# Performance work log

Measured on AMD Instinct MI355X. Metric: run time of the kernel, lower is better.

The kernel has to match this reference:

```python
import jax, jax.numpy as jnp
import numpy as np
import math

CTX_LEN = 2048
N_EMB = 256
HEAD_SIZE = 256
N_HEADS = 8
HEAD_DIM = HEAD_SIZE // N_HEADS  # 32
B, T = 4, 2048


def setup_inputs() -> dict:
    key = jax.random.key(0)
    k1, k2, k3, k4 = jax.random.split(key, 4)
    x = jax.random.normal(k1, (B, T, N_EMB), dtype=jnp.float32)
    # torch Linear(n_emb, 3*head_size, bias=False): store as [in, out] for x @ W
    w_attn = jax.random.normal(k2, (N_EMB, 3 * HEAD_SIZE), dtype=jnp.float32) * 0.02
    pos_embs = jax.random.normal(k3, (N_HEADS, CTX_LEN, HEAD_DIM), dtype=jnp.float32) * 0.02
    w_proj = jax.random.normal(k4, (HEAD_SIZE, N_EMB), dtype=jnp.float32) * 0.02
    b_proj = jnp.zeros((N_EMB,), dtype=jnp.float32)
    return {"x": x, "w_attn": w_attn, "pos_embs": pos_embs,
            "w_proj": w_proj, "b_proj": b_proj}


def reference(x, w_attn, pos_embs, w_proj, b_proj):
    Bsz, Tlen, _ = x.shape
    qkv = x @ w_attn                               # [B,T,3*HS]
    K, Q, V = jnp.split(qkv, 3, axis=-1)           # split order: K, Q, V (as in source)
    def heads(t):                                  # [B,T,HS] -> [B,H,T,hd]
        return t.reshape(Bsz, Tlen, N_HEADS, HEAD_DIM).transpose(0, 2, 1, 3)
    K, Q, V = heads(K), heads(Q), heads(V)

    # relative position term with skew trick
    pe = pos_embs[:, -Tlen:, :]                    # [H,T,hd]
    S_rel = jnp.einsum('bhtd,hsd->bhts', Q, pe)    # [B,H,T,T]
    flip_mask = jnp.flip(jnp.tril(jnp.ones((Tlen, Tlen), dtype=x.dtype)), axis=1)
    S_rel = S_rel * flip_mask
    # pad a zero column at the front, reshape [T+1,T], drop first row -> skew
    S_rel = jnp.pad(S_rel, ((0, 0), (0, 0), (0, 0), (1, 0)))
    S_rel = S_rel.reshape(Bsz, N_HEADS, Tlen + 1, Tlen)[:, :, 1:, :]

    scores = (jnp.einsum('bhtd,bhsd->bhts', Q, K) + S_rel) / math.sqrt(HEAD_DIM)
    causal = jnp.where(jnp.tril(jnp.ones((Tlen, Tlen), dtype=bool)), 0.0, -1e9).astype(x.dtype)
    scores = scores + causal
    attn = jax.nn.softmax(scores, axis=-1)         # dropout omitted (eval mode)

    out = jnp.einsum('bhts,bhsd->bhtd', attn, V)   # [B,H,T,hd]
    out = out.transpose(0, 2, 1, 3).reshape(Bsz, Tlen, HEAD_SIZE)
    return out @ w_proj + b_proj
```

## Files before the change

kernel.cpp:

```cpp
#include <hip/hip_runtime.h>
#include <math.h>

#define BB 4
#define TT 2048
#define TTP 2112
#define NEMB 256
#define NH 8
#define HD 32

typedef __attribute__((ext_vector_type(8))) short bf8;
typedef __attribute__((ext_vector_type(4))) float f4;

static __device__ __forceinline__ unsigned short f2bf(float f) {
    union { float f; unsigned u; } v; v.f = f;
    unsigned r = v.u + 0x7FFF + ((v.u >> 16) & 1);
    return (unsigned short)(r >> 16);
}
static __device__ __forceinline__ float bf2f(unsigned short s) {
    union { unsigned u; float f; } v; v.u = ((unsigned)s) << 16;
    return v.f;
}

template <int CTRL>
static __device__ __forceinline__ float dppmv(float x) {
    return __int_as_float(__builtin_amdgcn_mov_dpp(__float_as_int(x), CTRL, 0xF, 0xF, true));
}
static __device__ __forceinline__ float rowsum16(float x) {
    x += dppmv<0xB1>(x);
    x += dppmv<0x4E>(x);
    x += dppmv<0x124>(x);
    x += dppmv<0x128>(x);
    return x;
}

static __device__ __forceinline__ void tcvt_body(const float* __restrict__ src,
                                                 unsigned short* __restrict__ dst,
                                                 int R, int C, int gx, int gy,
                                                 float (*t)[65], int tid) {
    const int c0 = gx * 64, r0 = gy * 64;
    #pragma unroll
    for (int p = 0; p < 4; ++p) {
        const int i = tid + p * 256;
        const int r = i >> 4, c4 = (i & 15) * 4;
        const float4 v = *(const float4*)(src + (long)(r0 + r) * C + c0 + c4);
        t[r][c4] = v.x; t[r][c4+1] = v.y; t[r][c4+2] = v.z; t[r][c4+3] = v.w;
    }
    __syncthreads();
    #pragma unroll
    for (int p = 0; p < 4; ++p) {
        const int i = tid + p * 256;
        const int cr = i >> 4, r4 = (i & 15) * 4;
        ushort4 vv;
        vv.x = f2bf(t[r4+0][cr]); vv.y = f2bf(t[r4+1][cr]);
        vv.z = f2bf(t[r4+2][cr]); vv.w = f2bf(t[r4+3][cr]);
        *(ushort4*)(dst + (long)(c0 + cr) * R + r0 + r4) = vv;
    }
}

__global__ __launch_bounds__(256) void prep(const float* __restrict__ pe,
                                            unsigned short* __restrict__ peb,
                                            const float* __restrict__ wa,
                                            unsigned short* __restrict__ waT,
                                            const float* __restrict__ wp,
                                            unsigned short* __restrict__ wpT) {
    __shared__ float t[64][65];
    const int bx = blockIdx.x, tid = threadIdx.x;
    if (bx < 528) {
        const int idx4 = bx * 256 + tid;
        const int h   = idx4 / 16896;
        const int rem = idx4 - h * 16896;
        const int u   = rem >> 3;
        const int d4  = (rem & 7) * 4;
        ushort4 o = make_ushort4(0, 0, 0, 0);
        if (u < TT) {
            const float4 v = *(const float4*)(pe + ((long)(h * TT + u)) * HD + d4);
            o.x = f2bf(v.x); o.y = f2bf(v.y); o.z = f2bf(v.z); o.w = f2bf(v.w);
        }
        *(ushort4*)(peb + ((long)(h * TTP + u)) * HD + d4) = o;
    } else if (bx < 576) {
        const int lo = bx - 528;
        tcvt_body(wa, waT, 256, 768, lo % 12, lo / 12, t, tid);
    } else {
        const int lo = bx - 576;
        tcvt_body(wp, wpT, 256, 256, lo % 4, lo / 4, t, tid);
    }
}

__global__ __launch_bounds__(256) void qkv_mfma(const float* __restrict__ xg,
                                                const unsigned short* __restrict__ Bg,
                                                unsigned short* __restrict__ Kb,
                                                unsigned short* __restrict__ Qb,
                                                unsigned short* __restrict__ Vt) {
    __shared__ unsigned short sm[13824];
    unsigned short* As = sm;
    unsigned short* Bs = sm + 9216;
    const int tid = threadIdx.x;
    const int wv = tid >> 6, L = tid & 63;
    const int l15 = L & 15, q = L >> 4;
    const int n0 = blockIdx.x * 64;
    const int m0 = blockIdx.y * 128;

    f4 acc[2][4];
    #pragma unroll
    for (int mt = 0; mt < 2; ++mt)
        #pragma unroll
        for (int nt = 0; nt < 4; ++nt) acc[mt][nt] = (f4){0.f,0.f,0.f,0.f};

    for (int kc = 0; kc < 4; ++kc) {
        const int k0 = kc * 64;
        __syncthreads();
        #pragma unroll
        for (int p = 0; p < 4; ++p) {
            const int i = tid + p * 256;
            const int r = i >> 3, c = i & 7;
            const float4 va = *(const float4*)(xg + (long)(m0 + r) * 256 + k0 + c * 8);
            const float4 vb = *(const float4*)(xg + (long)(m0 + r) * 256 + k0 + c * 8 + 4);
            ushort4 lo, hi;
            lo.x = f2bf(va.x); lo.y = f2bf(va.y); lo.z = f2bf(va.z); lo.w = f2bf(va.w);
            hi.x = f2bf(vb.x); hi.y = f2bf(vb.y); hi.z = f2bf(vb.z); hi.w = f2bf(vb.w);
            *(ushort4*)(As + r * 72 + c * 8)     = lo;
            *(ushort4*)(As + r * 72 + c * 8 + 4) = hi;
        }
        #pragma unroll
        for (int p = 0; p < 2; ++p) {
            const int i = tid + p * 256;
            const int r = i >> 3, c = i & 7;
            *(bf8*)(Bs + r * 72 + c * 8) = *(const bf8*)(Bg + (long)(n0 + r) * 256 + k0 + c * 8);
        }
        __syncthreads();
        #pragma unroll
        for (int kk = 0; kk < 2; ++kk) {
            const bf8 a0 = *(const bf8*)(As + (wv * 32 + l15) * 72 + kk * 32 + q * 8);
            const bf8 a1 = *(const bf8*)(As + (wv * 32 + 16 + l15) * 72 + kk * 32 + q * 8);
            #pragma unroll
            for (int nt = 0; nt < 4; ++nt) {
                const bf8 bb = *(const bf8*)(Bs + (nt * 16 + l15) * 72 + kk * 32 + q * 8);
                acc[0][nt] = __builtin_amdgcn_mfma_f32_16x16x32_bf16(a0, bb, acc[0][nt], 0, 0, 0);
                acc[1][nt] = __builtin_amdgcn_mfma_f32_16x16x32_bf16(a1, bb, acc[1][nt], 0, 0, 0);
            }
        }
    }

    const int sec = n0 >> 8;
    #pragma unroll
    for (int mt = 0; mt < 2; ++mt) {
        const int gm = m0 + wv * 32 + mt * 16 + q * 4;
        const int b = gm >> 11, tb = gm & 2047;
        #pragma unroll
        for (int nt = 0; nt < 4; ++nt) {
            const int gn = n0 + nt * 16 + l15;
            const int cc = gn & 255, h = cc >> 5, d = cc & 31;
            const long bh = (long)b * NH + h;
            const f4 a = acc[mt][nt];
            if (sec == 2) {
                ushort4 vv;
                vv.x = f2bf(a[0]); vv.y = f2bf(a[1]); vv.z = f2bf(a[2]); vv.w = f2bf(a[3]);
                *(ushort4*)(Vt + (bh * HD + d) * TT + tb) = vv;
            } else if (sec == 1) {
                #pragma unroll
                for (int r = 0; r < 4; ++r)
                    Qb[(bh * TT + tb + r) * HD + d] = f2bf(a[r] * 0.25506655788696527f);
            } else {
                #pragma unroll
                for (int r = 0; r < 4; ++r)
                    Kb[(bh * TT + tb + r) * HD + d] = f2bf(a[r]);
            }
        }
    }
}

__global__ __launch_bounds__(256) void attn_kernel(const unsigned short* __restrict__ Kb,
                                                   const unsigned short* __restrict__ Qb,
                                                   const unsigned short* __restrict__ Vtg,
                                                   const unsigned short* __restrict__ peb,
                                                   unsigned short* __restrict__ po,
                                                   float* __restrict__ pl) {
    __shared__ unsigned short lds[14592];
    unsigned short* Ks  = lds;
    unsigned short* PEs = lds + 2560;
    unsigned short* Vts = lds + 7680;
    unsigned short* Psw = lds + 9984 + (threadIdx.x >> 6) * 1152;

    const int tid = threadIdx.x;
    const int wv  = tid >> 6;
    const int L   = tid & 63;
    const int l15 = L & 15;
    const int q   = L >> 4;
    const int pair = blockIdx.x >> 1;
    const int sblk = blockIdx.x & 1;
    const int h = blockIdx.y, b = blockIdx.z;
    const long bh = (long)b * NH + h;
    const unsigned short* Kg = Kb  + bh * TT * HD;
    const unsigned short* Qg = Qb  + bh * TT * HD;
    const unsigned short* Vg = Vtg + bh * HD * TT;
    const unsigned short* Pg = peb + (long)h * TTP * HD;

    const int krow = tid >> 2, kc = tid & 3;
    const int vrow = tid >> 3, vc = tid & 7;
    const f4 z4 = {0.f, 0.f, 0.f, 0.f};
    const f4 m4 = {-16.f, -16.f, -16.f, -16.f};

    int saddr[4]; unsigned psel[4];
    #pragma unroll
    for (int r = 0; r < 4; ++r) {
        const int tcol = l15 + 15 - 4 * q - r;
        saddr[r] = ((q << 4) | (tcol & 15)) << 2;
        psel[r]  = (tcol < 16) ? 0x01000C0Cu : 0x03020C0Cu;
    }

    for (int half = 0; half < 2; ++half) {
        const int itile = half ? 31 - pair : pair;
        const int t0 = itile * 64;

        const bf8 aq = *(const bf8*)(Qg + (t0 + wv * 16 + l15) * HD + q * 8);
        f4 o0 = z4, o1 = z4;
        float l_st[4] = {0.f, 0.f, 0.f, 0.f};

        for (int jt = sblk; jt <= itile; jt += 2) {
            const int s0 = jt * 64;
            const int ubase = TT - 64 - t0 + s0;
            __syncthreads();
            *(bf8*)(Ks  + krow * 40 + kc * 8) = *(const bf8*)(Kg + (s0 + krow) * HD + kc * 8);
            *(bf8*)(Vts + vrow * 72 + vc * 8) = *(const bf8*)(Vg + vrow * TT + s0 + vc * 8);
            #pragma unroll
            for (int kk = 0; kk < 2; ++kk) {
                const int i  = tid + kk * 256;
                const int pr = i >> 2, pc = i & 3;
                *(bf8*)(PEs + pr * 40 + pc * 8) = *(const bf8*)(Pg + (long)(ubase + pr) * HD + pc * 8);
            }
            __syncthreads();

            f4 sa[4], ra[5];
            #pragma unroll
            for (int nt = 0; nt < 4; ++nt) {
                const bf8 bk = *(const bf8*)(Ks + (nt * 16 + l15) * 40 + q * 8);
                sa[nt] = __builtin_amdgcn_mfma_f32_16x16x32_bf16(aq, bk, m4, 0, 0, 0);
            }
            const int pebase = 48 - 16 * wv;
            #pragma unroll
            for (int nt = 0; nt < 5; ++nt) {
                const bf8 bp = *(const bf8*)(PEs + (pebase + nt * 16 + l15) * 40 + q * 8);
                ra[nt] = __builtin_amdgcn_mfma_f32_16x16x32_bf16(aq, bp, z4, 0, 0, 0);
            }

            #pragma unroll
            for (int nb = 0; nb < 4; ++nb) {
                #pragma unroll
                for (int r = 0; r < 4; ++r) {
                    const unsigned packed = __builtin_amdgcn_perm(
                        (unsigned)__float_as_int(ra[nb + 1][r]),
                        (unsigned)__float_as_int(ra[nb][r]), 0x07060302u);
                    const int v = __builtin_amdgcn_ds_bpermute(saddr[r], (int)packed);
                    const unsigned sel = __builtin_amdgcn_perm((unsigned)v, (unsigned)v, psel[r]);
                    sa[nb][r] += __int_as_float((int)sel);
                }
            }

            if (jt == itile) {
                #pragma unroll
                for (int nb = 0; nb < 4; ++nb)
                    #pragma unroll
                    for (int r = 0; r < 4; ++r) {
                        const int s_l = nb * 16 + l15;
                        const int t_l = wv * 16 + 4 * q + r;
                        if (s_l > t_l) sa[nb][r] = -1e30f;
                    }
            }

            #pragma unroll
            for (int r = 0; r < 4; ++r) {
                #pragma unroll
                for (int nb = 0; nb < 4; ++nb) {
                    const float p = exp2f(sa[nb][r]);
                    l_st[r] += p;
                    const unsigned pu = (unsigned)__float_as_int(p);
                    Psw[(4 * q + r) * 72 + nb * 16 + l15] =
                        (unsigned short)((pu + 0x8000u) >> 16);
                }
            }

            #pragma unroll
            for (int ks = 0; ks < 2; ++ks) {
                const bf8 ap  = *(const bf8*)(Psw + l15 * 72 + ks * 32 + q * 8);
                const bf8 bv0 = *(const bf8*)(Vts + l15 * 72 + ks * 32 + q * 8);
                const bf8 bv1 = *(const bf8*)(Vts + (16 + l15) * 72 + ks * 32 + q * 8);
                o0 = __builtin_amdgcn_mfma_f32_16x16x32_bf16(ap, bv0, o0, 0, 0, 0);
                o1 = __builtin_amdgcn_mfma_f32_16x16x32_bf16(ap, bv1, o1, 0, 0, 0);
            }
        }

        const long pt = (bh * 32 + itile) * 2 + sblk;
        unsigned short* pob = po + pt * 2048;
        #pragma unroll
        for (int r = 0; r < 4; ++r) {
            const int row = wv * 16 + 4 * q + r;
            pob[row * 32 + l15]      = f2bf(o0[r]);
            pob[row * 32 + 16 + l15] = f2bf(o1[r]);
            const float ls = rowsum16(l_st[r]);
            if (l15 == 0) pl[pt * 64 + row] = ls;
        }
    }
}

__global__ __launch_bounds__(256) void attn_merge(const unsigned short* __restrict__ po,
                                                  const float* __restrict__ pl,
                                                  unsigned short* __restrict__ attb) {
    const int i = blockIdx.x * 256 + threadIdx.x;
    const int d4   = i & 7;
    const int row  = (i >> 3) & 63;
    const int tile = (i >> 9) & 31;
    const int bh   = i >> 14;
    const int h = bh & 7, b = bh >> 3;
    const long pt0 = ((long)bh * 32 + tile) * 2;
    const float l0 = pl[pt0 * 64 + row], l1 = pl[(pt0 + 1) * 64 + row];
    const float inv = 1.0f / (l0 + l1);
    const ushort4 a = *(const ushort4*)(po + pt0 * 2048 + row * 32 + d4 * 4);
    const ushort4 c = *(const ushort4*)(po + (pt0 + 1) * 2048 + row * 32 + d4 * 4);
    ushort4 o;
    o.x = f2bf((bf2f(a.x) + bf2f(c.x)) * inv);
    o.y = f2bf((bf2f(a.y) + bf2f(c.y)) * inv);
    o.z = f2bf((bf2f(a.z) + bf2f(c.z)) * inv);
    o.w = f2bf((bf2f(a.w) + bf2f(c.w)) * inv);
    const int t = tile * 64 + row;
    *(ushort4*)(attb + ((long)(b * TT + t)) * NEMB + h * HD + d4 * 4) = o;
}

__global__ __launch_bounds__(256) void proj_mfma(const unsigned short* __restrict__ Ag,
                                                 const unsigned short* __restrict__ Bg,
                                                 const float* __restrict__ bias,
                                                 float* __restrict__ out) {
    __shared__ unsigned short sm[13824];
    unsigned short* As = sm;
    unsigned short* Bs = sm + 9216;
    const int tid = threadIdx.x;
    const int wv = tid >> 6, L = tid & 63;
    const int l15 = L & 15, q = L >> 4;
    const int n0 = blockIdx.x * 64;
    const int m0 = blockIdx.y * 128;

    f4 acc[2][4];
    #pragma unroll
    for (int mt = 0; mt < 2; ++mt)
        #pragma unroll
        for (int nt = 0; nt < 4; ++nt) acc[mt][nt] = (f4){0.f,0.f,0.f,0.f};

    for (int kc = 0; kc < 4; ++kc) {
        const int k0 = kc * 64;
        __syncthreads();
        #pragma unroll
        for (int p = 0; p < 4; ++p) {
            const int i = tid + p * 256;
            const int r = i >> 3, c = i & 7;
            *(bf8*)(As + r * 72 + c * 8) = *(const bf8*)(Ag + (long)(m0 + r) * 256 + k0 + c * 8);
        }
        #pragma unroll
        for (int p = 0; p < 2; ++p) {
            const int i = tid + p * 256;
            const int r = i >> 3, c = i & 7;
            *(bf8*)(Bs + r * 72 + c * 8) = *(const bf8*)(Bg + (long)(n0 + r) * 256 + k0 + c * 8);
        }
        __syncthreads();
        #pragma unroll
        for (int kk = 0; kk < 2; ++kk) {
            const bf8 a0 = *(const bf8*)(As + (wv * 32 + l15) * 72 + kk * 32 + q * 8);
            const bf8 a1 = *(const bf8*)(As + (wv * 32 + 16 + l15) * 72 + kk * 32 + q * 8);
            #pragma unroll
            for (int nt = 0; nt < 4; ++nt) {
                const bf8 bb = *(const bf8*)(Bs + (nt * 16 + l15) * 72 + kk * 32 + q * 8);
                acc[0][nt] = __builtin_amdgcn_mfma_f32_16x16x32_bf16(a0, bb, acc[0][nt], 0, 0, 0);
                acc[1][nt] = __builtin_amdgcn_mfma_f32_16x16x32_bf16(a1, bb, acc[1][nt], 0, 0, 0);
            }
        }
    }

    #pragma unroll
    for (int mt = 0; mt < 2; ++mt) {
        const int gm = m0 + wv * 32 + mt * 16 + q * 4;
        #pragma unroll
        for (int nt = 0; nt < 4; ++nt) {
            const int gn = n0 + nt * 16 + l15;
            const float bv = bias[gn];
            #pragma unroll
            for (int r = 0; r < 4; ++r)
                out[(long)(gm + r) * NEMB + gn] = acc[mt][nt][r] + bv;
        }
    }
}

extern "C" void kernel_launch(void* const* d_in, const int* in_sizes, int n_in,
                              void* d_out, int out_size, void* d_ws, size_t ws_size,
                              hipStream_t stream) {
    const float* x      = (const float*)d_in[0];
    const float* w_attn = (const float*)d_in[1];
    const float* pe     = (const float*)d_in[2];
    const float* w_proj = (const float*)d_in[3];
    const float* b_proj = (const float*)d_in[4];
    float* out = (float*)d_out;

    char* base = (char*)d_ws;
    unsigned short* Kb   = (unsigned short*)(base);
    unsigned short* Qb   = (unsigned short*)(base + ( 4u << 20));
    unsigned short* Vt   = (unsigned short*)(base + ( 8u << 20));
    unsigned short* attb = (unsigned short*)(base + (12u << 20));
    unsigned short* peb  = (unsigned short*)(base + (16u << 20));
    unsigned short* waT  = (unsigned short*)(base + (18u << 20));
    unsigned short* wpT  = (unsigned short*)(base + (37u << 19));
    unsigned short* po   = (unsigned short*)(base + (19u << 20));
    float*          pl   = (float*)        (base + (27u << 20));

    prep<<<dim3(592), 256, 0, stream>>>(pe, peb, w_attn, waT, w_proj, wpT);
    qkv_mfma<<<dim3(12, 64), 256, 0, stream>>>(x, waT, Kb, Qb, Vt);
    attn_kernel<<<dim3(32, NH, BB), 256, 0, stream>>>(Kb, Qb, Vt, peb, po, pl);
    attn_merge<<<dim3(2048), 256, 0, stream>>>(po, pl, attb);
    proj_mfma<<<dim3(4, 64), 256, 0, stream>>>(attb, wpT, b_proj, out);
}
```

Measured before the change: 153.8 us.

## Process both paired query tiles in one KV sweep, sharing K/V tile loads

The attention kernel now handles its two query tiles (pair and 31-pair) in a single loop over key tiles instead of two sequential passes. Each K/V tile is loaded into LDS once and used by both query tiles, with a separate positional-embedding buffer for each. This halves K/V global loads and the number of barrier-separated iterations. The skew shuffle is also reworked to issue 3 ds_bpermute per row instead of 4, and the P scratch stride changes from 72 to 76. The cost is more LDS per block and extra registers for the second set of accumulators, which may reduce occupancy.

```diff
diff --git a/kernel.cpp b/kernel.cpp
--- a/kernel.cpp
+++ b/kernel.cpp
@@ -169,17 +169,83 @@
     }
 }
 
+
+static __device__ __forceinline__ void finish_tile(
+    f4* sa, const bf8 aq, const unsigned short* __restrict__ PEs,
+    unsigned short* __restrict__ Psw, bool diag,
+    const bf8 bv00, const bf8 bv01, const bf8 bv10, const bf8 bv11,
+    f4& o0, f4& o1, float* l_st,
+    const int* saddr, const unsigned* pselL, const unsigned* pselX,
+    int wv, int l15, int q)
+{
+    const f4 z4 = {0.f, 0.f, 0.f, 0.f};
+    const int pebase = 48 - 16 * wv;
+    f4 ra[5];
+    #pragma unroll
+    for (int nt = 0; nt < 5; ++nt) {
+        const bf8 bp = *(const bf8*)(PEs + (pebase + nt * 16 + l15) * 40 + q * 8);
+        ra[nt] = __builtin_amdgcn_mfma_f32_16x16x32_bf16(aq, bp, z4, 0, 0, 0);
+    }
+
+    #pragma unroll
+    for (int r = 0; r < 4; ++r) {
+        const unsigned w0 = __builtin_amdgcn_perm(
+            (unsigned)__float_as_int(ra[1][r]), (unsigned)__float_as_int(ra[0][r]), 0x07060302u);
+        const unsigned w1 = __builtin_amdgcn_perm(
+            (unsigned)__float_as_int(ra[3][r]), (unsigned)__float_as_int(ra[2][r]), 0x07060302u);
+        const unsigned w2 = ((unsigned)__float_as_int(ra[4][r])) >> 16;
+        const int v0 = __builtin_amdgcn_ds_bpermute(saddr[r], (int)w0);
+        const int v1 = __builtin_amdgcn_ds_bpermute(saddr[r], (int)w1);
+        const int v2 = __builtin_amdgcn_ds_bpermute(saddr[r], (int)w2);
+        sa[0][r] += __int_as_float((int)__builtin_amdgcn_perm((unsigned)v0, (unsigned)v0, pselL[r]));
+        sa[1][r] += __int_as_float((int)__builtin_amdgcn_perm((unsigned)v1, (unsigned)v0, pselX[r]));
+        sa[2][r] += __int_as_float((int)__builtin_amdgcn_perm((unsigned)v1, (unsigned)v1, pselL[r]));
+        sa[3][r] += __int_as_float((int)__builtin_amdgcn_perm((unsigned)v2, (unsigned)v1, pselX[r]));
+    }
+
+    if (diag) {
+        #pragma unroll
+        for (int nb = 0; nb < 4; ++nb)
+            #pragma unroll
+            for (int r = 0; r < 4; ++r) {
+                const int s_l = nb * 16 + l15;
+                const int t_l = wv * 16 + 4 * q + r;
+                if (s_l > t_l) sa[nb][r] = -1e30f;
+            }
+    }
+
+    #pragma unroll
+    for (int r = 0; r < 4; ++r) {
+        #pragma unroll
+        for (int nb = 0; nb < 4; ++nb) {
+            const float p = exp2f(sa[nb][r]);
+            l_st[r] += p;
+            const unsigned pu = (unsigned)__float_as_int(p);
+            Psw[(4 * q + r) * 76 + nb * 16 + l15] =
+                (unsigned short)((pu + 0x8000u) >> 16);
+        }
+    }
+
+    #pragma unroll
+    for (int ks = 0; ks < 2; ++ks) {
+        const bf8 ap = *(const bf8*)(Psw + l15 * 76 + ks * 32 + q * 8);
+        o0 = __builtin_amdgcn_mfma_f32_16x16x32_bf16(ap, ks ? bv10 : bv00, o0, 0, 0, 0);
+        o1 = __builtin_amdgcn_mfma_f32_16x16x32_bf16(ap, ks ? bv11 : bv01, o1, 0, 0, 0);
+    }
+}
+
 __global__ __launch_bounds__(256) void attn_kernel(const unsigned short* __restrict__ Kb,
                                                    const unsigned short* __restrict__ Qb,
                                                    const unsigned short* __restrict__ Vtg,
                                                    const unsigned short* __restrict__ peb,
                                                    unsigned short* __restrict__ po,
                                                    float* __restrict__ pl) {
-    __shared__ unsigned short lds[14592];
-    unsigned short* Ks  = lds;
-    unsigned short* PEs = lds + 2560;
-    unsigned short* Vts = lds + 7680;
-    unsigned short* Psw = lds + 9984 + (threadIdx.x >> 6) * 1152;
+    __shared__ unsigned short lds[19968];
+    unsigned short* Ks   = lds;
+    unsigned short* PEsB = lds + 2560;
+    unsigned short* PEsA = lds + 7680;
+    unsigned short* Vts  = lds + 12800;
+    unsigned short* Psw  = lds + 15104 + (threadIdx.x >> 6) * 1216;
 
     const int tid = threadIdx.x;
     const int wv  = tid >> 6;
@@ -200,103 +266,91 @@
     const f4 z4 = {0.f, 0.f, 0.f, 0.f};
     const f4 m4 = {-16.f, -16.f, -16.f, -16.f};
 
-    int saddr[4]; unsigned psel[4];
+    int saddr[4]; unsigned pselL[4], pselX[4];
     #pragma unroll
     for (int r = 0; r < 4; ++r) {
         const int tcol = l15 + 15 - 4 * q - r;
         saddr[r] = ((q << 4) | (tcol & 15)) << 2;
-        psel[r]  = (tcol < 16) ? 0x01000C0Cu : 0x03020C0Cu;
-    }
-
-    for (int half = 0; half < 2; ++half) {
-        const int itile = half ? 31 - pair : pair;
-        const int t0 = itile * 64;
-
-        const bf8 aq = *(const bf8*)(Qg + (t0 + wv * 16 + l15) * HD + q * 8);
-        f4 o0 = z4, o1 = z4;
-        float l_st[4] = {0.f, 0.f, 0.f, 0.f};
-
-        for (int jt = sblk; jt <= itile; jt += 2) {
-            const int s0 = jt * 64;
-            const int ubase = TT - 64 - t0 + s0;
-            __syncthreads();
-            *(bf8*)(Ks  + krow * 40 + kc * 8) = *(const bf8*)(Kg + (s0 + krow) * HD + kc * 8);
-            *(bf8*)(Vts + vrow * 72 + vc * 8) = *(const bf8*)(Vg + vrow * TT + s0 + vc * 8);
+        const bool c = tcol >= 16;
+        pselL[r] = c ? 0x03020C0Cu : 0x01000C0Cu;
+        pselX[r] = c ? 0x05040C0Cu : 0x03020C0Cu;
+    }
+
+    const int iA = pair, iB = 31 - pair;
+    const int t0A = iA * 64, t0B = iB * 64;
+
+    const bf8 aqA = *(const bf8*)(Qg + (t0A + wv * 16 + l15) * HD + q * 8);
+    const bf8 aqB = *(const bf8*)(Qg + (t0B + wv * 16 + l15) * HD + q * 8);
+
+    f4 oA0 = z4, oA1 = z4, oB0 = z4, oB1 = z4;
+    float lA[4] = {0.f, 0.f, 0.f, 0.f}, lB[4] = {0.f, 0.f, 0.f, 0.f};
+
+    for (int jt = sblk; jt <= iB; jt += 2) {
+        const int s0 = jt * 64;
+        const bool actA = (jt <= iA);
+        __syncthreads();
+        *(bf8*)(Ks  + krow * 40 + kc * 8) = *(const bf8*)(Kg + (s0 + krow) * HD + kc * 8);
+        *(bf8*)(Vts + vrow * 72 + vc * 8) = *(const bf8*)(Vg + vrow * TT + s0 + vc * 8);
+        const int ubB = TT - 64 - t0B + s0;
+        #pragma unroll
+        for (int kk = 0; kk < 2; ++kk) {
+            const int i  = tid + kk * 256;
+            const int pr = i >> 2, pc = i & 3;
+            *(bf8*)(PEsB + pr * 40 + pc * 8) = *(const bf8*)(Pg + (long)(ubB + pr) * HD + pc * 8);
+        }
+        if (actA) {
+            const int ubA = TT - 64 - t0A + s0;
             #pragma unroll
             for (int kk = 0; kk < 2; ++kk) {
                 const int i  = tid + kk * 256;
                 const int pr = i >> 2, pc = i & 3;
-                *(bf8*)(PEs + pr * 40 + pc * 8) = *(const bf8*)(Pg + (long)(ubase + pr) * HD + pc * 8);
+                *(bf8*)(PEsA + pr * 40 + pc * 8) = *(const bf8*)(Pg + (long)(ubA + pr) * HD + pc * 8);
             }
-            __syncthreads();
-
-            f4 sa[4], ra[5];
-            #pragma unroll
-            for (int nt = 0; nt < 4; ++nt) {
-                const bf8 bk = *(const bf8*)(Ks + (nt * 16 + l15) * 40 + q * 8);
-                sa[nt] = __builtin_amdgcn_mfma_f32_16x16x32_bf16(aq, bk, m4, 0, 0, 0);
-            }
-            const int pebase = 48 - 16 * wv;
-            #pragma unroll
-            for (int nt = 0; nt < 5; ++nt) {
-                const bf8 bp = *(const bf8*)(PEs + (pebase + nt * 16 + l15) * 40 + q * 8);
-                ra[nt] = __builtin_amdgcn_mfma_f32_16x16x32_bf16(aq, bp, z4, 0, 0, 0);
-            }
-
-            #pragma unroll
-            for (int nb = 0; nb < 4; ++nb) {
-                #pragma unroll
-                for (int r = 0; r < 4; ++r) {
-                    const unsigned packed = __builtin_amdgcn_perm(
-                        (unsigned)__float_as_int(ra[nb + 1][r]),
-                        (unsigned)__float_as_int(ra[nb][r]), 0x07060302u);
-                    const int v = __builtin_amdgcn_ds_bpermute(saddr[r], (int)packed);
-                    const unsigned sel = __builtin_amdgcn_perm((unsigned)v, (unsigned)v, psel[r]);
-                    sa[nb][r] += __int_as_float((int)sel);
-                }
-            }
-
-            if (jt == itile) {
-                #pragma unroll
-                for (int nb = 0; nb < 4; ++nb)
-                    #pragma unroll
-                    for (int r = 0; r < 4; ++r) {
-                        const int s_l = nb * 16 + l15;
-                        const int t_l = wv * 16 + 4 * q + r;
-                        if (s_l > t_l) sa[nb][r] = -1e30f;
-                    }
-            }
-
-            #pragma unroll
-            for (int r = 0; r < 4; ++r) {
-                #pragma unroll
-                for (int nb = 0; nb < 4; ++nb) {
-                    const float p = exp2f(sa[nb][r]);
-                    l_st[r] += p;
-                    const unsigned pu = (unsigned)__float_as_int(p);
-                    Psw[(4 * q + r) * 72 + nb * 16 + l15] =
-                        (unsigned short)((pu + 0x8000u) >> 16);
-                }
-            }
-
-            #pragma unroll
-            for (int ks = 0; ks < 2; ++ks) {
-                const bf8 ap  = *(const bf8*)(Psw + l15 * 72 + ks * 32 + q * 8);
-                const bf8 bv0 = *(const bf8*)(Vts + l15 * 72 + ks * 32 + q * 8);
-                const bf8 bv1 = *(const bf8*)(Vts + (16 + l15) * 72 + ks * 32 + q * 8);
-                o0 = __builtin_amdgcn_mfma_f32_16x16x32_bf16(ap, bv0, o0, 0, 0, 0);
-                o1 = __builtin_amdgcn_mfma_f32_16x16x32_bf16(ap, bv1, o1, 0, 0, 0);
-            }
-        }
-
-        const long pt = (bh * 32 + itile) * 2 + sblk;
+        }
+        __syncthreads();
+
+        f4 saA[4], saB[4];
+        #pragma unroll
+        for (int nt = 0; nt < 4; ++nt) {
+            const bf8 bk = *(const bf8*)(Ks + (nt * 16 + l15) * 40 + q * 8);
+            saB[nt] = __builtin_amdgcn_mfma_f32_16x16x32_bf16(aqB, bk, m4, 0, 0, 0);
+            if (actA)
+                saA[nt] = __builtin_amdgcn_mfma_f32_16x16x32_bf16(aqA, bk, m4, 0, 0, 0);
+        }
+
+        const bf8 bv00 = *(const bf8*)(Vts + l15 * 72 + q * 8);
+        const bf8 bv01 = *(const bf8*)(Vts + (16 + l15) * 72 + q * 8);
+        const bf8 bv10 = *(const bf8*)(Vts + l15 * 72 + 32 + q * 8);
+        const bf8 bv11 = *(const bf8*)(Vts + (16 + l15) * 72 + 32 + q * 8);
+
+        finish_tile(saB, aqB, PEsB, Psw, jt == iB, bv00, bv01, bv10, bv11,
+                    oB0, oB1, lB, saddr, pselL, pselX, wv, l15, q);
+        if (actA)
+            finish_tile(saA, aqA, PEsA, Psw, jt == iA, bv00, bv01, bv10, bv11,
+                        oA0, oA1, lA, saddr, pselL, pselX, wv, l15, q);
+    }
+
+    {
+        const long pt = (bh * 32 + iB) * 2 + sblk;
         unsigned short* pob = po + pt * 2048;
         #pragma unroll
         for (int r = 0; r < 4; ++r) {
             const int row = wv * 16 + 4 * q + r;
-            pob[row * 32 + l15]      = f2bf(o0[r]);
-            pob[row * 32 + 16 + l15] = f2bf(o1[r]);
-            const float ls = rowsum16(l_st[r]);
+            pob[row * 32 + l15]      = f2bf(oB0[r]);
+            pob[row * 32 + 16 + l15] = f2bf(oB1[r]);
+            const float ls = rowsum16(lB[r]);
+            if (l15 == 0) pl[pt * 64 + row] = ls;
+        }
+    }
+    {
+        const long pt = (bh * 32 + iA) * 2 + sblk;
+        unsigned short* pob = po + pt * 2048;
+        #pragma unroll
+        for (int r = 0; r < 4; ++r) {
+            const int row = wv * 16 + 4 * q + r;
+            pob[row * 32 + l15]      = f2bf(oA0[r]);
+            pob[row * 32 + 16 + l15] = f2bf(oA1[r]);
+            const float ls = rowsum16(lA[r]);
             if (l15 == 0) pl[pt * 64 + row] = ls;
         }
     }
```

Result: slower. 162.8 us (+5.9%).

## Prefetch next K/V/PE tile into registers and cut bpermutes in skew

Applied to the files above, without the earlier changes.

Global loads for the next key tile (K, transposed V and two position-embedding slabs) are now issued right after the barrier into registers and stored to LDS at the start of the following iteration. This software-pipelines global memory latency behind the MFMA and softmax work of the current tile. The relative-position skew now packs the five ra results into three words, issuing 12 ds_bpermute calls per tile instead of 16, with two byte-select masks. The per-wave P staging stride changes from 72 to 76 halves to reduce LDS bank conflicts, though this breaks 16-byte alignment of the bf8 reads and adds register pressure.

```diff
diff --git a/kernel.cpp b/kernel.cpp
--- a/kernel.cpp
+++ b/kernel.cpp
@@ -175,11 +175,11 @@
                                                    const unsigned short* __restrict__ peb,
                                                    unsigned short* __restrict__ po,
                                                    float* __restrict__ pl) {
-    __shared__ unsigned short lds[14592];
+    __shared__ unsigned short lds[14848];
     unsigned short* Ks  = lds;
     unsigned short* PEs = lds + 2560;
     unsigned short* Vts = lds + 7680;
-    unsigned short* Psw = lds + 9984 + (threadIdx.x >> 6) * 1152;
+    unsigned short* Psw = lds + 9984 + (threadIdx.x >> 6) * 1216;
 
     const int tid = threadIdx.x;
     const int wv  = tid >> 6;
@@ -200,12 +200,14 @@
     const f4 z4 = {0.f, 0.f, 0.f, 0.f};
     const f4 m4 = {-16.f, -16.f, -16.f, -16.f};
 
-    int saddr[4]; unsigned psel[4];
+    int saddr[4]; unsigned pselL[4], pselX[4];
     #pragma unroll
     for (int r = 0; r < 4; ++r) {
         const int tcol = l15 + 15 - 4 * q - r;
         saddr[r] = ((q << 4) | (tcol & 15)) << 2;
-        psel[r]  = (tcol < 16) ? 0x01000C0Cu : 0x03020C0Cu;
+        const bool c = tcol >= 16;
+        pselL[r] = c ? 0x03020C0Cu : 0x01000C0Cu;
+        pselX[r] = c ? 0x05040C0Cu : 0x03020C0Cu;
     }
 
     for (int half = 0; half < 2; ++half) {
@@ -216,19 +218,32 @@
         f4 o0 = z4, o1 = z4;
         float l_st[4] = {0.f, 0.f, 0.f, 0.f};
 
+        bf8 ck, cv, cp0, cp1;
+        if (sblk <= itile) {
+            const int s0 = sblk * 64;
+            const int ub = TT - 64 - t0 + s0;
+            ck  = *(const bf8*)(Kg + (s0 + krow) * HD + kc * 8);
+            cv  = *(const bf8*)(Vg + vrow * TT + s0 + vc * 8);
+            cp0 = *(const bf8*)(Pg + (long)(ub + krow) * HD + kc * 8);
+            cp1 = *(const bf8*)(Pg + (long)(ub + 64 + krow) * HD + kc * 8);
+        }
+
         for (int jt = sblk; jt <= itile; jt += 2) {
-            const int s0 = jt * 64;
-            const int ubase = TT - 64 - t0 + s0;
             __syncthreads();
-            *(bf8*)(Ks  + krow * 40 + kc * 8) = *(const bf8*)(Kg + (s0 + krow) * HD + kc * 8);
-            *(bf8*)(Vts + vrow * 72 + vc * 8) = *(const bf8*)(Vg + vrow * TT + s0 + vc * 8);
-            #pragma unroll
-            for (int kk = 0; kk < 2; ++kk) {
-                const int i  = tid + kk * 256;
-                const int pr = i >> 2, pc = i & 3;
-                *(bf8*)(PEs + pr * 40 + pc * 8) = *(const bf8*)(Pg + (long)(ubase + pr) * HD + pc * 8);
-            }
+            *(bf8*)(Ks  + krow * 40 + kc * 8)        = ck;
+            *(bf8*)(Vts + vrow * 72 + vc * 8)        = cv;
+            *(bf8*)(PEs + krow * 40 + kc * 8)        = cp0;
+            *(bf8*)(PEs + (krow + 64) * 40 + kc * 8) = cp1;
             __syncthreads();
+
+            if (jt + 2 <= itile) {
+                const int s0n = (jt + 2) * 64;
+                const int ubn = TT - 64 - t0 + s0n;
+                ck  = *(const bf8*)(Kg + (s0n + krow) * HD + kc * 8);
+                cv  = *(const bf8*)(Vg + vrow * TT + s0n + vc * 8);
+                cp0 = *(const bf8*)(Pg + (long)(ubn + krow) * HD + kc * 8);
+                cp1 = *(const bf8*)(Pg + (long)(ubn + 64 + krow) * HD + kc * 8);
+            }
 
             f4 sa[4], ra[5];
             #pragma unroll
@@ -244,16 +259,19 @@
             }
 
             #pragma unroll
-            for (int nb = 0; nb < 4; ++nb) {
-                #pragma unroll
-                for (int r = 0; r < 4; ++r) {
-                    const unsigned packed = __builtin_amdgcn_perm(
-                        (unsigned)__float_as_int(ra[nb + 1][r]),
-                        (unsigned)__float_as_int(ra[nb][r]), 0x07060302u);
-                    const int v = __builtin_amdgcn_ds_bpermute(saddr[r], (int)packed);
-                    const unsigned sel = __builtin_amdgcn_perm((unsigned)v, (unsigned)v, psel[r]);
-                    sa[nb][r] += __int_as_float((int)sel);
-                }
+            for (int r = 0; r < 4; ++r) {
+                const unsigned w0 = __builtin_amdgcn_perm(
+                    (unsigned)__float_as_int(ra[1][r]), (unsigned)__float_as_int(ra[0][r]), 0x07060302u);
+                const unsigned w1 = __builtin_amdgcn_perm(
+                    (unsigned)__float_as_int(ra[3][r]), (unsigned)__float_as_int(ra[2][r]), 0x07060302u);
+                const unsigned w2 = ((unsigned)__float_as_int(ra[4][r])) >> 16;
+                const int v0 = __builtin_amdgcn_ds_bpermute(saddr[r], (int)w0);
+                const int v1 = __builtin_amdgcn_ds_bpermute(saddr[r], (int)w1);
+                const int v2 = __builtin_amdgcn_ds_bpermute(saddr[r], (int)w2);
+                sa[0][r] += __int_as_float((int)__builtin_amdgcn_perm((unsigned)v0, (unsigned)v0, pselL[r]));
+                sa[1][r] += __int_as_float((int)__builtin_amdgcn_perm((unsigned)v1, (unsigned)v0, pselX[r]));
+                sa[2][r] += __int_as_float((int)__builtin_amdgcn_perm((unsigned)v1, (unsigned)v1, pselL[r]));
+                sa[3][r] += __int_as_float((int)__builtin_amdgcn_perm((unsigned)v2, (unsigned)v1, pselX[r]));
             }
 
             if (jt == itile) {
@@ -274,14 +292,14 @@
                     const float p = exp2f(sa[nb][r]);
                     l_st[r] += p;
                     const unsigned pu = (unsigned)__float_as_int(p);
-                    Psw[(4 * q + r) * 72 + nb * 16 + l15] =
+                    Psw[(4 * q + r) * 76 + nb * 16 + l15] =
                         (unsigned short)((pu + 0x8000u) >> 16);
                 }
             }
 
             #pragma unroll
             for (int ks = 0; ks < 2; ++ks) {
-                const bf8 ap  = *(const bf8*)(Psw + l15 * 72 + ks * 32 + q * 8);
+                const bf8 ap  = *(const bf8*)(Psw + l15 * 76 + ks * 32 + q * 8);
                 const bf8 bv0 = *(const bf8*)(Vts + l15 * 72 + ks * 32 + q * 8);
                 const bf8 bv1 = *(const bf8*)(Vts + (16 + l15) * 72 + ks * 32 + q * 8);
                 o0 = __builtin_amdgcn_mfma_f32_16x16x32_bf16(ap, bv0, o0, 0, 0, 0);
```

Measured after the change: 156.2 us. About the same (+1.6%).

## Fuse attention merge into projection GEMM and pre-convert x to bf16

Applied to the files above, without the earlier changes.

Removes the separate attn_merge kernel by having proj_mfma combine the two partial attention outputs and normalise them while it loads its A tile. This saves one launch and a round-trip of the bf16 attention buffer. It also moves the fp32-to-bf16 conversion of x out of qkv_mfma into extra blocks of prep, so x is converted once rather than once per N-block (12 times). The cost is an extra write and read of bf16 x, and proj_mfma now redoes the merge arithmetic for each of its 4 N-blocks.

```diff
diff --git a/kernel.cpp b/kernel.cpp
--- a/kernel.cpp
+++ b/kernel.cpp
@@ -62,7 +62,9 @@
                                             const float* __restrict__ wa,
                                             unsigned short* __restrict__ waT,
                                             const float* __restrict__ wp,
-                                            unsigned short* __restrict__ wpT) {
+                                            unsigned short* __restrict__ wpT,
+                                            const float* __restrict__ x,
+                                            unsigned short* __restrict__ xb) {
     __shared__ float t[64][65];
     const int bx = blockIdx.x, tid = threadIdx.x;
     if (bx < 528) {
@@ -80,13 +82,19 @@
     } else if (bx < 576) {
         const int lo = bx - 528;
         tcvt_body(wa, waT, 256, 768, lo % 12, lo / 12, t, tid);
-    } else {
+    } else if (bx < 592) {
         const int lo = bx - 576;
         tcvt_body(wp, wpT, 256, 256, lo % 4, lo / 4, t, tid);
-    }
-}
-
-__global__ __launch_bounds__(256) void qkv_mfma(const float* __restrict__ xg,
+    } else {
+        const long xi = ((long)(bx - 592) * 256 + tid) * 4;
+        const float4 v = *(const float4*)(x + xi);
+        ushort4 o;
+        o.x = f2bf(v.x); o.y = f2bf(v.y); o.z = f2bf(v.z); o.w = f2bf(v.w);
+        *(ushort4*)(xb + xi) = o;
+    }
+}
+
+__global__ __launch_bounds__(256) void qkv_mfma(const unsigned short* __restrict__ Ag,
                                                 const unsigned short* __restrict__ Bg,
                                                 unsigned short* __restrict__ Kb,
                                                 unsigned short* __restrict__ Qb,
@@ -113,13 +121,7 @@
         for (int p = 0; p < 4; ++p) {
             const int i = tid + p * 256;
             const int r = i >> 3, c = i & 7;
-            const float4 va = *(const float4*)(xg + (long)(m0 + r) * 256 + k0 + c * 8);
-            const float4 vb = *(const float4*)(xg + (long)(m0 + r) * 256 + k0 + c * 8 + 4);
-            ushort4 lo, hi;
-            lo.x = f2bf(va.x); lo.y = f2bf(va.y); lo.z = f2bf(va.z); lo.w = f2bf(va.w);
-            hi.x = f2bf(vb.x); hi.y = f2bf(vb.y); hi.z = f2bf(vb.z); hi.w = f2bf(vb.w);
-            *(ushort4*)(As + r * 72 + c * 8)     = lo;
-            *(ushort4*)(As + r * 72 + c * 8 + 4) = hi;
+            *(bf8*)(As + r * 72 + c * 8) = *(const bf8*)(Ag + (long)(m0 + r) * 256 + k0 + c * 8);
         }
         #pragma unroll
         for (int p = 0; p < 2; ++p) {
@@ -302,30 +304,8 @@
     }
 }
 
-__global__ __launch_bounds__(256) void attn_merge(const unsigned short* __restrict__ po,
-                                                  const float* __restrict__ pl,
-                                                  unsigned short* __restrict__ attb) {
-    const int i = blockIdx.x * 256 + threadIdx.x;
-    const int d4   = i & 7;
-    const int row  = (i >> 3) & 63;
-    const int tile = (i >> 9) & 31;
-    const int bh   = i >> 14;
-    const int h = bh & 7, b = bh >> 3;
-    const long pt0 = ((long)bh * 32 + tile) * 2;
-    const float l0 = pl[pt0 * 64 + row], l1 = pl[(pt0 + 1) * 64 + row];
-    const float inv = 1.0f / (l0 + l1);
-    const ushort4 a = *(const ushort4*)(po + pt0 * 2048 + row * 32 + d4 * 4);
-    const ushort4 c = *(const ushort4*)(po + (pt0 + 1) * 2048 + row * 32 + d4 * 4);
-    ushort4 o;
-    o.x = f2bf((bf2f(a.x) + bf2f(c.x)) * inv);
-    o.y = f2bf((bf2f(a.y) + bf2f(c.y)) * inv);
-    o.z = f2bf((bf2f(a.z) + bf2f(c.z)) * inv);
-    o.w = f2bf((bf2f(a.w) + bf2f(c.w)) * inv);
-    const int t = tile * 64 + row;
-    *(ushort4*)(attb + ((long)(b * TT + t)) * NEMB + h * HD + d4 * 4) = o;
-}
-
-__global__ __launch_bounds__(256) void proj_mfma(const unsigned short* __restrict__ Ag,
+__global__ __launch_bounds__(256) void proj_mfma(const unsigned short* __restrict__ po,
+                                                 const float* __restrict__ pl,
                                                  const unsigned short* __restrict__ Bg,
                                                  const float* __restrict__ bias,
                                                  float* __restrict__ out) {
@@ -351,7 +331,31 @@
         for (int p = 0; p < 4; ++p) {
             const int i = tid + p * 256;
             const int r = i >> 3, c = i & 7;
-            *(bf8*)(As + r * 72 + c * 8) = *(const bf8*)(Ag + (long)(m0 + r) * 256 + k0 + c * 8);
+            const int gm = m0 + r;
+            const int b = gm >> 11, t = gm & 2047;
+            const int tile = t >> 6, row = t & 63;
+            const int k = k0 + c * 8;
+            const int h = k >> 5, d0 = k & 31;
+            const long pt0 = (((long)b * NH + h) * 32 + tile) * 2;
+            const float l0 = pl[pt0 * 64 + row], l1 = pl[(pt0 + 1) * 64 + row];
+            const float inv = 1.0f / (l0 + l1);
+            const unsigned short* p0 = po + pt0 * 2048 + row * 32 + d0;
+            const unsigned short* p1 = p0 + 2048;
+            ushort4 o0, o1;
+            const ushort4 a0 = *(const ushort4*)(p0);
+            const ushort4 b0 = *(const ushort4*)(p1);
+            const ushort4 a1 = *(const ushort4*)(p0 + 4);
+            const ushort4 b1 = *(const ushort4*)(p1 + 4);
+            o0.x = f2bf((bf2f(a0.x) + bf2f(b0.x)) * inv);
+            o0.y = f2bf((bf2f(a0.y) + bf2f(b0.y)) * inv);
+            o0.z = f2bf((bf2f(a0.z) + bf2f(b0.z)) * inv);
+            o0.w = f2bf((bf2f(a0.w) + bf2f(b0.w)) * inv);
+            o1.x = f2bf((bf2f(a1.x) + bf2f(b1.x)) * inv);
+            o1.y = f2bf((bf2f(a1.y) + bf2f(b1.y)) * inv);
+            o1.z = f2bf((bf2f(a1.z) + bf2f(b1.z)) * inv);
+            o1.w = f2bf((bf2f(a1.w) + bf2f(b1.w)) * inv);
+            *(ushort4*)(As + r * 72 + c * 8)     = o0;
+            *(ushort4*)(As + r * 72 + c * 8 + 4) = o1;
         }
         #pragma unroll
         for (int p = 0; p < 2; ++p) {
@@ -401,16 +405,15 @@
     unsigned short* Kb   = (unsigned short*)(base);
     unsigned short* Qb   = (unsigned short*)(base + ( 4u << 20));
     unsigned short* Vt   = (unsigned short*)(base + ( 8u << 20));
-    unsigned short* attb = (unsigned short*)(base + (12u << 20));
+    unsigned short* xb   = (unsigned short*)(base + (12u << 20));
     unsigned short* peb  = (unsigned short*)(base + (16u << 20));
     unsigned short* waT  = (unsigned short*)(base + (18u << 20));
     unsigned short* wpT  = (unsigned short*)(base + (37u << 19));
     unsigned short* po   = (unsigned short*)(base + (19u << 20));
     float*          pl   = (float*)        (base + (27u << 20));
 
-    prep<<<dim3(592), 256, 0, stream>>>(pe, peb, w_attn, waT, w_proj, wpT);
-    qkv_mfma<<<dim3(12, 64), 256, 0, stream>>>(x, waT, Kb, Qb, Vt);
+    prep<<<dim3(2640), 256, 0, stream>>>(pe, peb, w_attn, waT, w_proj, wpT, x, xb);
+    qkv_mfma<<<dim3(12, 64), 256, 0, stream>>>(xb, waT, Kb, Qb, Vt);
     attn_kernel<<<dim3(32, NH, BB), 256, 0, stream>>>(Kb, Qb, Vt, peb, po, pl);
-    attn_merge<<<dim3(2048), 256, 0, stream>>>(po, pl, attb);
-    proj_mfma<<<dim3(4, 64), 256, 0, stream>>>(attb, wpT, b_proj, out);
-}
+    proj_mfma<<<dim3(4, 64), 256, 0, stream>>>(po, pl, wpT, b_proj, out);
+}
```

After: 149.5 us. 1.03x faster.
